# Optimization experiments

Measured on AMD Instinct MI355X. Metric: run time of the kernel, lower is better.

Reference implementation:

```python
import jax, jax.numpy as jnp
import numpy as np

L = 16       # flow_layers
B = 131072   # batch
D = 256      # z_dim
EPS = 1e-7


def setup_inputs() -> dict:
    key = jax.random.key(0)
    ks = jax.random.split(key, 7)
    z = jax.random.normal(ks[0], (B, D), dtype=jnp.float32)
    # match torch init ranges
    planar_w = jax.random.uniform(ks[1], (L, D), jnp.float32, -0.01, 0.01)
    planar_b = jax.random.uniform(ks[2], (L,), jnp.float32, -0.01, 0.01)
    planar_s = jax.random.uniform(ks[3], (L, D), jnp.float32, -0.01, 0.01)
    radial_z0 = jax.random.uniform(ks[4], (L, D), jnp.float32, -0.01, 0.01)
    radial_a = jax.random.uniform(ks[5], (L,), jnp.float32, 0.01, 1.0)
    radial_b = jax.random.uniform(ks[6], (L,), jnp.float32, -0.01, 0.01)
    return dict(z=z, planar_w=planar_w, planar_b=planar_b, planar_s=planar_s,
                radial_z0=radial_z0, radial_a=radial_a, radial_b=radial_b)


def reference(z, planar_w, planar_b, planar_s, radial_z0, radial_a, radial_b):
    # Faithful translation of AlternatingFlow._run_flow with train=True.
    # The torch .item() parameter corrections become predicated jnp.where updates.
    loss = jnp.zeros((z.shape[0],), dtype=z.dtype)
    for i in range(L):
        if i % 2 == 0:  # planar flow step
            w = planar_w[i]          # [D]
            b = planar_b[i]          # scalar
            s = planar_s[i]          # [D]
            margin = jnp.dot(s, w)   # scalar  (mm(scale, weight.T))
            comp = -1.0 + jnp.log1p(jnp.exp(margin)) - margin
            s = jnp.where(margin < -1.0, s + comp * w / jnp.linalg.norm(w), s)
            act = jnp.tanh(z @ w + b)                 # [B]
            z = z + s[None, :] * act[:, None]          # [B, D]
            psi_dot_s = (1.0 - act * act) * jnp.dot(w, s)  # psi @ s.T, [B]
            det = 1.0 + psi_dot_s
            loss = loss + jnp.log(jnp.abs(det) + EPS)
        else:  # radial flow step
            z0 = radial_z0[i]        # [D]
            a = radial_a[i]          # scalar
            beta = radial_b[i]       # scalar
            beta = jnp.where(beta < -a, -a + jnp.log1p(jnp.exp(beta)), beta)
            radius = z - z0[None, :]                   # [B, D]
            r = jnp.linalg.norm(radius, axis=1)        # [B], per-row norm
            h = 1.0 / (a + r)                          # [B]
            z = z + beta * h[:, None] * radius
            # NOTE: torch uses radius.norm(2) with no dim here -> scalar full-tensor norm
            R = jnp.linalg.norm(radius)                # scalar (faithful to original)
            diagonal = (1.0 + beta * h) ** (D - 1)
            det = diagonal * (1.0 + beta * h - beta * (h * h) * R)
            loss = loss + jnp.log(jnp.abs(det) + EPS)
    return z, jnp.mean(loss)
```

## Files before the change

kernel.cpp:

```cpp
#include <hip/hip_runtime.h>
#include <hip/hip_fp16.h>
#include <math.h>

#define B_ROWS 131072
#define DDIM 256
#define EPSF 1e-7f
#define NB1 4096
#define NWAVES (NB1 * 8)
#define NB3 512

#define PBW_OFF  0
#define RV_OFF   1179648
#define PL_OFF   1179712
#define PBRL_OFF 1179776
#define HW_OFF   1183872

__device__ __forceinline__ float uni(float x) {
    return __int_as_float(__builtin_amdgcn_readfirstlane(__float_as_int(x)));
}

#define DPP_ADD(v, ctrl)                                                        \
    (v) += __int_as_float(__builtin_amdgcn_update_dpp(                          \
               0, __float_as_int(v), (ctrl), 0xF, 0xF, true))

#define REDUCE16(v)                                                             \
    do {                                                                        \
        DPP_ADD(v, 0xB1);                             \
        DPP_ADD(v, 0x4E);                             \
        DPP_ADD(v, 0x124);                            \
        DPP_ADD(v, 0x128);                            \
    } while (0)

__global__ __launch_bounds__(512, 6) void k_main(
    const float* __restrict__ z_in, float* __restrict__ z_out,
    const float* __restrict__ pw, const float* __restrict__ pb,
    const float* __restrict__ ps, const float* __restrict__ rz0,
    const float* __restrict__ ra, const float* __restrict__ rb,
    __half* __restrict__ h_ws, float* __restrict__ pbw)
{
    __shared__ float swp[8 * DDIM];
    __shared__ float ssp[8 * DDIM];
    __shared__ float sz0[8 * DDIM];
    __shared__ float sscal[32];

    const int wave = threadIdx.x >> 6;
    const int lane = threadIdx.x & 63;

    {
        const int p = wave;
        const int ip = 2 * p, ir = 2 * p + 1;
        float4 wv  = ((const float4*)(pw  + ip * DDIM))[lane];
        float4 sv  = ((const float4*)(ps  + ip * DDIM))[lane];
        float4 z0v = ((const float4*)(rz0 + ir * DDIM))[lane];
        float m  = wv.x * sv.x + wv.y * sv.y + wv.z * sv.z + wv.w * sv.w;
        float n2 = wv.x * wv.x + wv.y * wv.y + wv.z * wv.z + wv.w * wv.w;
#pragma unroll
        for (int o = 1; o < 64; o <<= 1) {
            m  += __shfl_xor(m,  o, 64);
            n2 += __shfl_xor(n2, o, 64);
        }
        if (m < -1.0f) {
            float comp = -1.0f + log1pf(expf(m)) - m;
            float f = comp / sqrtf(n2);
            sv.x += f * wv.x; sv.y += f * wv.y; sv.z += f * wv.z; sv.w += f * wv.w;
        }
        float wd = wv.x * sv.x + wv.y * sv.y + wv.z * sv.z + wv.w * sv.w;
#pragma unroll
        for (int o = 1; o < 64; o <<= 1) wd += __shfl_xor(wd, o, 64);
        const int nd = ((lane & 3) << 6) | ((lane >> 2) << 2);
        *((float4*)(swp + p * DDIM + nd)) = wv;
        *((float4*)(ssp + p * DDIM + nd)) = sv;
        *((float4*)(sz0 + p * DDIM + nd)) = z0v;
        if (lane == 0) {
            sscal[p]      = pb[ip];
            sscal[8 + p]  = wd;
            float a = ra[ir], bt = rb[ir];
            if (bt < -a) bt = -a + log1pf(expf(bt));
            sscal[16 + p] = a;
            sscal[24 + p] = bt;
        }
    }
    __syncthreads();

    float pbv[8], wds[8], av[8], bv[8];
#pragma unroll
    for (int p = 0; p < 8; ++p) {
        pbv[p] = uni(sscal[p]);
        wds[p] = uni(sscal[8 + p]);
        av[p]  = uni(sscal[16 + p]);
        bv[p]  = uni(sscal[24 + p]);
    }

    const int g = lane >> 4;
    const int j = lane & 15;
    const int row = blockIdx.x * 32 + wave * 4 + g;

    float4 zv[4];
    {
        const float4* zp = (const float4*)(z_in + (size_t)row * DDIM + j * 16);
#pragma unroll
        for (int k = 0; k < 4; ++k) zv[k] = zp[k];
    }

    float r2s[8];
    float pls = 0.0f;
    unsigned hw32[4];

#pragma unroll
    for (int i = 0; i < 16; ++i) {
        if ((i & 1) == 0) {
            const int p = i >> 1;
            const float4* wb = ((const float4*)swp) + p * 64 + j;
            float t = 0.0f;
#pragma unroll
            for (int k = 0; k < 4; ++k) {
                float4 wv = wb[k * 16];
                t += zv[k].x * wv.x + zv[k].y * wv.y + zv[k].z * wv.z + zv[k].w * wv.w;
            }
            REDUCE16(t);
            float x = t + pbv[p];
            float e = __expf(2.0f * x);
            float act = 1.0f - 2.0f / (e + 1.0f);
            const float4* sb = ((const float4*)ssp) + p * 64 + j;
#pragma unroll
            for (int k = 0; k < 4; ++k) {
                float4 sv = sb[k * 16];
                zv[k].x += sv.x * act; zv[k].y += sv.y * act;
                zv[k].z += sv.z * act; zv[k].w += sv.w * act;
            }
            float det = 1.0f + (1.0f - act * act) * wds[p];
            pls += __logf(fabsf(det) + EPSF);
        } else {
            const int r = i >> 1;
            const float4* zb = ((const float4*)sz0) + r * 64 + j;
            float4 rd[4];
            float t = 0.0f;
#pragma unroll
            for (int k = 0; k < 4; ++k) {
                float4 zz = zb[k * 16];
                rd[k].x = zv[k].x - zz.x; rd[k].y = zv[k].y - zz.y;
                rd[k].z = zv[k].z - zz.z; rd[k].w = zv[k].w - zz.w;
                t += rd[k].x * rd[k].x + rd[k].y * rd[k].y
                   + rd[k].z * rd[k].z + rd[k].w * rd[k].w;
            }
            REDUCE16(t);
            float rr = sqrtf(t);
            float h = 1.0f / (av[r] + rr);
            float bh = bv[r] * h;
#pragma unroll
            for (int k = 0; k < 4; ++k) {
                zv[k].x += bh * rd[k].x; zv[k].y += bh * rd[k].y;
                zv[k].z += bh * rd[k].z; zv[k].w += bh * rd[k].w;
            }
            r2s[r] = t;
            unsigned hu = (unsigned)__half_as_ushort(__float2half(h));
            if ((r & 1) == 0) hw32[r >> 1] = hu;
            else              hw32[r >> 1] |= hu << 16;
        }
    }

    {
        float4* op = (float4*)(z_out + (size_t)row * DDIM + j * 16);
#pragma unroll
        for (int k = 0; k < 4; ++k) op[k] = zv[k];
        if (j == 0)
            ((uint4*)h_ws)[row] = make_uint4(hw32[0], hw32[1], hw32[2], hw32[3]);
    }

    const int waveId = blockIdx.x * 8 + wave;
#pragma unroll
    for (int q = 0; q < 9; ++q) {
        float v = (q < 8) ? r2s[q] : pls;
        if (j != 0) v = 0.0f;
        v += __shfl_xor(v, 16, 64);
        v += __shfl_xor(v, 32, 64);
        if (lane == 0) pbw[waveId * 9 + q] = v;
    }
}

__global__ __launch_bounds__(1024) void k_stats(
    const float* __restrict__ pbw, double* __restrict__ Rv, double* __restrict__ PL)
{
    __shared__ double sd[1024];
    const int q = blockIdx.x;
    const int t = threadIdx.x;
    double v = 0.0;
    for (int i = t; i < NWAVES; i += 1024) v += (double)pbw[i * 9 + q];
    sd[t] = v;
    __syncthreads();
#pragma unroll
    for (int off = 512; off > 0; off >>= 1) {
        if (t < off) sd[t] += sd[t + off];
        __syncthreads();
    }
    if (t == 0) {
        if (q < 8) Rv[q] = sqrt(sd[0]);
        else       PL[0] = sd[0];
    }
}

__global__ __launch_bounds__(256) void k_rloss(
    const __half* __restrict__ h_ws, const float* __restrict__ ra,
    const float* __restrict__ rb, const double* __restrict__ Rv,
    double* __restrict__ pb_rl)
{
    __shared__ double sd[256];
    __shared__ float sbeta[8], sR[8];
    if (threadIdx.x < 8) {
        int r = threadIdx.x;
        float a = ra[2 * r + 1], bt = rb[2 * r + 1];
        if (bt < -a) bt = -a + log1pf(expf(bt));
        sbeta[r] = bt;
        sR[r] = (float)Rv[r];
    }
    __syncthreads();
    const int row = blockIdx.x * 256 + threadIdx.x;
    uint4 hp = ((const uint4*)h_ws)[row];
    unsigned hw[4] = {hp.x, hp.y, hp.z, hp.w};
    double ls = 0.0;
#pragma unroll
    for (int r = 0; r < 8; ++r) {
        unsigned hu = (hw[r >> 1] >> ((r & 1) * 16)) & 0xFFFFu;
        float h = __half2float(__ushort_as_half((unsigned short)hu));
        float beta = sbeta[r];
        float bh = beta * h;
        float t1 = 1.0f + bh;
        float diag = exp2f(255.0f * __log2f(t1));
        float det = diag * (t1 - beta * h * h * sR[r]);
        ls += (double)__logf(fabsf(det) + EPSF);
    }
    sd[threadIdx.x] = ls;
    __syncthreads();
#pragma unroll
    for (int off = 128; off > 0; off >>= 1) {
        if (threadIdx.x < off) sd[threadIdx.x] += sd[threadIdx.x + off];
        __syncthreads();
    }
    if (threadIdx.x == 0) pb_rl[blockIdx.x] = sd[0];
}

__global__ __launch_bounds__(256) void k_final(
    const double* __restrict__ pb_rl, const double* __restrict__ PL,
    float* __restrict__ out_loss)
{
    __shared__ double sd[256];
    int t = threadIdx.x;
    double v = 0.0;
    for (int jj = t; jj < NB3; jj += 256) v += pb_rl[jj];
    sd[t] = v;
    __syncthreads();
#pragma unroll
    for (int off = 128; off > 0; off >>= 1) {
        if (t < off) sd[t] += sd[t + off];
        __syncthreads();
    }
    if (t == 0) out_loss[0] = (float)((sd[0] + PL[0]) / (double)B_ROWS);
}

extern "C" void kernel_launch(void* const* d_in, const int* in_sizes, int n_in,
                              void* d_out, int out_size, void* d_ws, size_t ws_size,
                              hipStream_t stream) {
    const float* z   = (const float*)d_in[0];
    const float* pw  = (const float*)d_in[1];
    const float* pb  = (const float*)d_in[2];
    const float* ps  = (const float*)d_in[3];
    const float* rz0 = (const float*)d_in[4];
    const float* ra  = (const float*)d_in[5];
    const float* rb  = (const float*)d_in[6];
    float* out = (float*)d_out;

    char* ws = (char*)d_ws;
    float*  pbw   = (float*)(ws + PBW_OFF);
    double* Rv    = (double*)(ws + RV_OFF);
    double* PL    = (double*)(ws + PL_OFF);
    double* pb_rl = (double*)(ws + PBRL_OFF);
    __half* h_ws  = (__half*)(ws + HW_OFF);

    k_main<<<NB1, 512, 0, stream>>>(z, out, pw, pb, ps, rz0, ra, rb, h_ws, pbw);
    k_stats<<<9, 1024, 0, stream>>>(pbw, Rv, PL);
    k_rloss<<<NB3, 256, 0, stream>>>(h_ws, ra, rb, Rv, pb_rl);
    k_final<<<1, 256, 0, stream>>>(pb_rl, PL, out + (size_t)B_ROWS * DDIM);
}
```

Measured before the change: 98.32 us.

## Process two row tiles per block and use fast rcp/sqrt intrinsics

Halves the grid so each block handles 64 rows in two sequential tiles. This amortizes the per-block parameter setup (loading flow weights into shared memory, the margin corrections, the scalar broadcasts) over twice the rows, and halves the partial-sum buffer that the stats kernel reduces. It also swaps the exact division and sqrt for the hardware rcp/sqrt/rsq intrinsics and splits the dot products into four independent partial sums for more ILP. The cost is fewer blocks available to hide memory latency, plus slightly lower numerical precision.

```diff
diff --git a/kernel.cpp b/kernel.cpp
--- a/kernel.cpp
+++ b/kernel.cpp
@@ -5,15 +5,15 @@
 #define B_ROWS 131072
 #define DDIM 256
 #define EPSF 1e-7f
-#define NB1 4096
+#define NB1 2048
 #define NWAVES (NB1 * 8)
 #define NB3 512
 
 #define PBW_OFF  0
-#define RV_OFF   1179648
-#define PL_OFF   1179712
-#define PBRL_OFF 1179776
-#define HW_OFF   1183872
+#define RV_OFF   589824
+#define PL_OFF   589888
+#define PBRL_OFF 589952
+#define HW_OFF   594048
 
 __device__ __forceinline__ float uni(float x) {
     return __int_as_float(__builtin_amdgcn_readfirstlane(__float_as_int(x)));
@@ -30,6 +30,90 @@
         DPP_ADD(v, 0x124);                            \
         DPP_ADD(v, 0x128);                            \
     } while (0)
+
+#define TILE_BODY(ROWBASE)                                                      \
+    {                                                                           \
+        const int row = (ROWBASE) + wave * 4 + g;                               \
+        float4 zv[4];                                                           \
+        {                                                                       \
+            const float4* zp = (const float4*)(z_in + (size_t)row * DDIM + j * 16); \
+            _Pragma("unroll")                                                   \
+            for (int k = 0; k < 4; ++k) zv[k] = zp[k];                          \
+        }                                                                       \
+        float pls = 0.0f;                                                       \
+        unsigned hw32[4];                                                       \
+        _Pragma("unroll")                                                       \
+        for (int i = 0; i < 16; ++i) {                                          \
+            if ((i & 1) == 0) {                                     \
+                const int p = i >> 1;                                           \
+                const float4* wb = ((const float4*)swp) + p * 64 + j;           \
+                float t0, t1, t2, t3;                                           \
+                {                                                               \
+                    float4 w0 = wb[0], w1 = wb[16], w2 = wb[32], w3 = wb[48];   \
+                    t0 = zv[0].x * w0.x + zv[0].y * w0.y + zv[0].z * w0.z + zv[0].w * w0.w; \
+                    t1 = zv[1].x * w1.x + zv[1].y * w1.y + zv[1].z * w1.z + zv[1].w * w1.w; \
+                    t2 = zv[2].x * w2.x + zv[2].y * w2.y + zv[2].z * w2.z + zv[2].w * w2.w; \
+                    t3 = zv[3].x * w3.x + zv[3].y * w3.y + zv[3].z * w3.z + zv[3].w * w3.w; \
+                }                                                               \
+                float t = (t0 + t1) + (t2 + t3);                                \
+                REDUCE16(t);                                                    \
+                float x = t + pbv[p];                                           \
+                float e = __expf(2.0f * x);                                     \
+                float act = 1.0f - 2.0f * __builtin_amdgcn_rcpf(e + 1.0f);      \
+                const float4* sb = ((const float4*)ssp) + p * 64 + j;           \
+                _Pragma("unroll")                                               \
+                for (int k = 0; k < 4; ++k) {                                   \
+                    float4 sv = sb[k * 16];                                     \
+                    zv[k].x += sv.x * act; zv[k].y += sv.y * act;               \
+                    zv[k].z += sv.z * act; zv[k].w += sv.w * act;               \
+                }                                                               \
+                float det = 1.0f + (1.0f - act * act) * wds[p];                 \
+                pls += __logf(fabsf(det) + EPSF);                               \
+            } else {                                                \
+                const int r = i >> 1;                                           \
+                const float4* zb = ((const float4*)sz0) + r * 64 + j;           \
+                float4 rd[4];                                                   \
+                float t0, t1, t2, t3;                                           \
+                {                                                               \
+                    float4 z0 = zb[0], z1 = zb[16], z2 = zb[32], z3 = zb[48];   \
+                    rd[0].x = zv[0].x - z0.x; rd[0].y = zv[0].y - z0.y;         \
+                    rd[0].z = zv[0].z - z0.z; rd[0].w = zv[0].w - z0.w;         \
+                    rd[1].x = zv[1].x - z1.x; rd[1].y = zv[1].y - z1.y;         \
+                    rd[1].z = zv[1].z - z1.z; rd[1].w = zv[1].w - z1.w;         \
+                    rd[2].x = zv[2].x - z2.x; rd[2].y = zv[2].y - z2.y;         \
+                    rd[2].z = zv[2].z - z2.z; rd[2].w = zv[2].w - z2.w;         \
+                    rd[3].x = zv[3].x - z3.x; rd[3].y = zv[3].y - z3.y;         \
+                    rd[3].z = zv[3].z - z3.z; rd[3].w = zv[3].w - z3.w;         \
+                    t0 = rd[0].x * rd[0].x + rd[0].y * rd[0].y + rd[0].z * rd[0].z + rd[0].w * rd[0].w; \
+                    t1 = rd[1].x * rd[1].x + rd[1].y * rd[1].y + rd[1].z * rd[1].z + rd[1].w * rd[1].w; \
+                    t2 = rd[2].x * rd[2].x + rd[2].y * rd[2].y + rd[2].z * rd[2].z + rd[2].w * rd[2].w; \
+                    t3 = rd[3].x * rd[3].x + rd[3].y * rd[3].y + rd[3].z * rd[3].z + rd[3].w * rd[3].w; \
+                }                                                               \
+                float t = (t0 + t1) + (t2 + t3);                                \
+                REDUCE16(t);                                                    \
+                float rr = __builtin_amdgcn_sqrtf(t);                           \
+                float h = __builtin_amdgcn_rcpf(av[r] + rr);                    \
+                float bh = bv[r] * h;                                           \
+                _Pragma("unroll")                                               \
+                for (int k = 0; k < 4; ++k) {                                   \
+                    zv[k].x += bh * rd[k].x; zv[k].y += bh * rd[k].y;           \
+                    zv[k].z += bh * rd[k].z; zv[k].w += bh * rd[k].w;           \
+                }                                                               \
+                acc_ss[r] += (j == 0) ? t : 0.0f;                               \
+                unsigned hu = (unsigned)__half_as_ushort(__float2half(h));      \
+                if ((r & 1) == 0) hw32[r >> 1] = hu;                            \
+                else              hw32[r >> 1] |= hu << 16;                     \
+            }                                                                   \
+        }                                                                       \
+        acc_pl += (j == 0) ? pls : 0.0f;                                        \
+        {                                                                       \
+            float4* op = (float4*)(z_out + (size_t)row * DDIM + j * 16);        \
+            _Pragma("unroll")                                                   \
+            for (int k = 0; k < 4; ++k) op[k] = zv[k];                          \
+            if (j == 0)                                                         \
+                ((uint4*)h_ws)[row] = make_uint4(hw32[0], hw32[1], hw32[2], hw32[3]); \
+        }                                                                       \
+    }
 
 __global__ __launch_bounds__(512, 6) void k_main(
     const float* __restrict__ z_in, float* __restrict__ z_out,
@@ -61,7 +145,7 @@
         }
         if (m < -1.0f) {
             float comp = -1.0f + log1pf(expf(m)) - m;
-            float f = comp / sqrtf(n2);
+            float f = comp * __builtin_amdgcn_rsqf(n2);
             sv.x += f * wv.x; sv.y += f * wv.y; sv.z += f * wv.z; sv.w += f * wv.w;
         }
         float wd = wv.x * sv.x + wv.y * sv.y + wv.z * sv.z + wv.w * sv.w;
@@ -93,85 +177,20 @@
 
     const int g = lane >> 4;
     const int j = lane & 15;
-    const int row = blockIdx.x * 32 + wave * 4 + g;
-
-    float4 zv[4];
-    {
-        const float4* zp = (const float4*)(z_in + (size_t)row * DDIM + j * 16);
-#pragma unroll
-        for (int k = 0; k < 4; ++k) zv[k] = zp[k];
-    }
-
-    float r2s[8];
-    float pls = 0.0f;
-    unsigned hw32[4];
-
-#pragma unroll
-    for (int i = 0; i < 16; ++i) {
-        if ((i & 1) == 0) {
-            const int p = i >> 1;
-            const float4* wb = ((const float4*)swp) + p * 64 + j;
-            float t = 0.0f;
-#pragma unroll
-            for (int k = 0; k < 4; ++k) {
-                float4 wv = wb[k * 16];
-                t += zv[k].x * wv.x + zv[k].y * wv.y + zv[k].z * wv.z + zv[k].w * wv.w;
-            }
-            REDUCE16(t);
-            float x = t + pbv[p];
-            float e = __expf(2.0f * x);
-            float act = 1.0f - 2.0f / (e + 1.0f);
-            const float4* sb = ((const float4*)ssp) + p * 64 + j;
-#pragma unroll
-            for (int k = 0; k < 4; ++k) {
-                float4 sv = sb[k * 16];
-                zv[k].x += sv.x * act; zv[k].y += sv.y * act;
-                zv[k].z += sv.z * act; zv[k].w += sv.w * act;
-            }
-            float det = 1.0f + (1.0f - act * act) * wds[p];
-            pls += __logf(fabsf(det) + EPSF);
-        } else {
-            const int r = i >> 1;
-            const float4* zb = ((const float4*)sz0) + r * 64 + j;
-            float4 rd[4];
-            float t = 0.0f;
-#pragma unroll
-            for (int k = 0; k < 4; ++k) {
-                float4 zz = zb[k * 16];
-                rd[k].x = zv[k].x - zz.x; rd[k].y = zv[k].y - zz.y;
-                rd[k].z = zv[k].z - zz.z; rd[k].w = zv[k].w - zz.w;
-                t += rd[k].x * rd[k].x + rd[k].y * rd[k].y
-                   + rd[k].z * rd[k].z + rd[k].w * rd[k].w;
-            }
-            REDUCE16(t);
-            float rr = sqrtf(t);
-            float h = 1.0f / (av[r] + rr);
-            float bh = bv[r] * h;
-#pragma unroll
-            for (int k = 0; k < 4; ++k) {
-                zv[k].x += bh * rd[k].x; zv[k].y += bh * rd[k].y;
-                zv[k].z += bh * rd[k].z; zv[k].w += bh * rd[k].w;
-            }
-            r2s[r] = t;
-            unsigned hu = (unsigned)__half_as_ushort(__float2half(h));
-            if ((r & 1) == 0) hw32[r >> 1] = hu;
-            else              hw32[r >> 1] |= hu << 16;
-        }
-    }
-
-    {
-        float4* op = (float4*)(z_out + (size_t)row * DDIM + j * 16);
-#pragma unroll
-        for (int k = 0; k < 4; ++k) op[k] = zv[k];
-        if (j == 0)
-            ((uint4*)h_ws)[row] = make_uint4(hw32[0], hw32[1], hw32[2], hw32[3]);
-    }
+
+    float acc_ss[8];
+#pragma unroll
+    for (int q = 0; q < 8; ++q) acc_ss[q] = 0.0f;
+    float acc_pl = 0.0f;
+
+    const int rowbase = blockIdx.x * 64;
+    TILE_BODY(rowbase)
+    TILE_BODY(rowbase + 32)
 
     const int waveId = blockIdx.x * 8 + wave;
 #pragma unroll
     for (int q = 0; q < 9; ++q) {
-        float v = (q < 8) ? r2s[q] : pls;
-        if (j != 0) v = 0.0f;
+        float v = (q < 8) ? acc_ss[q] : acc_pl;
         v += __shfl_xor(v, 16, 64);
         v += __shfl_xor(v, 32, 64);
         if (lane == 0) pbw[waveId * 9 + q] = v;
```

Measured after the change: 111.7 us. 1.14x slower.

## Process two rows per lane group to reuse LDS parameter loads

Applied to the files above, without the earlier changes.

Each 16-lane group now carries two rows (A and B) through all 16 flow steps. This halves the number of blocks and the LDS reads of w, s and z0 per row, and gives two independent reduction chains for more instruction-level parallelism. It also switches to hardware rcp/rsq/sqrt intrinsics and lowers the occupancy hint to 4 blocks per CU to make room for the doubled register state. Workspace offsets are shrunk to match the halved wave count. Lower occupancy may hide memory latency less well, and the approximate intrinsics slightly change numerics.

```diff
diff --git a/kernel.cpp b/kernel.cpp
--- a/kernel.cpp
+++ b/kernel.cpp
@@ -5,15 +5,15 @@
 #define B_ROWS 131072
 #define DDIM 256
 #define EPSF 1e-7f
-#define NB1 4096
+#define NB1 2048
 #define NWAVES (NB1 * 8)
 #define NB3 512
 
 #define PBW_OFF  0
-#define RV_OFF   1179648
-#define PL_OFF   1179712
-#define PBRL_OFF 1179776
-#define HW_OFF   1183872
+#define RV_OFF   589824
+#define PL_OFF   589888
+#define PBRL_OFF 589952
+#define HW_OFF   594048
 
 __device__ __forceinline__ float uni(float x) {
     return __int_as_float(__builtin_amdgcn_readfirstlane(__float_as_int(x)));
@@ -31,7 +31,7 @@
         DPP_ADD(v, 0x128);                            \
     } while (0)
 
-__global__ __launch_bounds__(512, 6) void k_main(
+__global__ __launch_bounds__(512, 4) void k_main(
     const float* __restrict__ z_in, float* __restrict__ z_out,
     const float* __restrict__ pw, const float* __restrict__ pb,
     const float* __restrict__ ps, const float* __restrict__ rz0,
@@ -61,7 +61,7 @@
         }
         if (m < -1.0f) {
             float comp = -1.0f + log1pf(expf(m)) - m;
-            float f = comp / sqrtf(n2);
+            float f = comp * __builtin_amdgcn_rsqf(n2);
             sv.x += f * wv.x; sv.y += f * wv.y; sv.z += f * wv.z; sv.w += f * wv.w;
         }
         float wd = wv.x * sv.x + wv.y * sv.y + wv.z * sv.z + wv.w * sv.w;
@@ -93,85 +93,115 @@
 
     const int g = lane >> 4;
     const int j = lane & 15;
-    const int row = blockIdx.x * 32 + wave * 4 + g;
-
-    float4 zv[4];
+    const int rowA = blockIdx.x * 64 + wave * 8 + g;
+    const int rowB = rowA + 4;
+
+    float4 zvA[4], zvB[4];
     {
-        const float4* zp = (const float4*)(z_in + (size_t)row * DDIM + j * 16);
-#pragma unroll
-        for (int k = 0; k < 4; ++k) zv[k] = zp[k];
-    }
-
-    float r2s[8];
-    float pls = 0.0f;
-    unsigned hw32[4];
+        const float4* zpA = (const float4*)(z_in + (size_t)rowA * DDIM + j * 16);
+        const float4* zpB = (const float4*)(z_in + (size_t)rowB * DDIM + j * 16);
+#pragma unroll
+        for (int k = 0; k < 4; ++k) { zvA[k] = zpA[k]; zvB[k] = zpB[k]; }
+    }
+
+    float acc_ss[8];
+    float acc_pl = 0.0f;
+    unsigned hwA[4], hwB[4];
 
 #pragma unroll
     for (int i = 0; i < 16; ++i) {
         if ((i & 1) == 0) {
             const int p = i >> 1;
             const float4* wb = ((const float4*)swp) + p * 64 + j;
-            float t = 0.0f;
-#pragma unroll
-            for (int k = 0; k < 4; ++k) {
-                float4 wv = wb[k * 16];
-                t += zv[k].x * wv.x + zv[k].y * wv.y + zv[k].z * wv.z + zv[k].w * wv.w;
-            }
-            REDUCE16(t);
-            float x = t + pbv[p];
-            float e = __expf(2.0f * x);
-            float act = 1.0f - 2.0f / (e + 1.0f);
+            float4 w0 = wb[0], w1 = wb[16], w2 = wb[32], w3 = wb[48];
+            float tA0 = zvA[0].x * w0.x + zvA[0].y * w0.y + zvA[0].z * w0.z + zvA[0].w * w0.w;
+            float tB0 = zvB[0].x * w0.x + zvB[0].y * w0.y + zvB[0].z * w0.z + zvB[0].w * w0.w;
+            float tA1 = zvA[1].x * w1.x + zvA[1].y * w1.y + zvA[1].z * w1.z + zvA[1].w * w1.w;
+            float tB1 = zvB[1].x * w1.x + zvB[1].y * w1.y + zvB[1].z * w1.z + zvB[1].w * w1.w;
+            float tA2 = zvA[2].x * w2.x + zvA[2].y * w2.y + zvA[2].z * w2.z + zvA[2].w * w2.w;
+            float tB2 = zvB[2].x * w2.x + zvB[2].y * w2.y + zvB[2].z * w2.z + zvB[2].w * w2.w;
+            float tA3 = zvA[3].x * w3.x + zvA[3].y * w3.y + zvA[3].z * w3.z + zvA[3].w * w3.w;
+            float tB3 = zvB[3].x * w3.x + zvB[3].y * w3.y + zvB[3].z * w3.z + zvB[3].w * w3.w;
+            float tA = (tA0 + tA1) + (tA2 + tA3);
+            float tB = (tB0 + tB1) + (tB2 + tB3);
+            REDUCE16(tA);
+            REDUCE16(tB);
+            float xA = tA + pbv[p], xB = tB + pbv[p];
+            float eA = __expf(2.0f * xA), eB = __expf(2.0f * xB);
+            float actA = 1.0f - 2.0f * __builtin_amdgcn_rcpf(eA + 1.0f);
+            float actB = 1.0f - 2.0f * __builtin_amdgcn_rcpf(eB + 1.0f);
             const float4* sb = ((const float4*)ssp) + p * 64 + j;
-#pragma unroll
-            for (int k = 0; k < 4; ++k) {
-                float4 sv = sb[k * 16];
-                zv[k].x += sv.x * act; zv[k].y += sv.y * act;
-                zv[k].z += sv.z * act; zv[k].w += sv.w * act;
-            }
-            float det = 1.0f + (1.0f - act * act) * wds[p];
-            pls += __logf(fabsf(det) + EPSF);
+            float4 s0 = sb[0], s1 = sb[16], s2 = sb[32], s3 = sb[48];
+            zvA[0].x += s0.x * actA; zvA[0].y += s0.y * actA; zvA[0].z += s0.z * actA; zvA[0].w += s0.w * actA;
+            zvB[0].x += s0.x * actB; zvB[0].y += s0.y * actB; zvB[0].z += s0.z * actB; zvB[0].w += s0.w * actB;
+            zvA[1].x += s1.x * actA; zvA[1].y += s1.y * actA; zvA[1].z += s1.z * actA; zvA[1].w += s1.w * actA;
+            zvB[1].x += s1.x * actB; zvB[1].y += s1.y * actB; zvB[1].z += s1.z * actB; zvB[1].w += s1.w * actB;
+            zvA[2].x += s2.x * actA; zvA[2].y += s2.y * actA; zvA[2].z += s2.z * actA; zvA[2].w += s2.w * actA;
+            zvB[2].x += s2.x * actB; zvB[2].y += s2.y * actB; zvB[2].z += s2.z * actB; zvB[2].w += s2.w * actB;
+            zvA[3].x += s3.x * actA; zvA[3].y += s3.y * actA; zvA[3].z += s3.z * actA; zvA[3].w += s3.w * actA;
+            zvB[3].x += s3.x * actB; zvB[3].y += s3.y * actB; zvB[3].z += s3.z * actB; zvB[3].w += s3.w * actB;
+            float detA = 1.0f + (1.0f - actA * actA) * wds[p];
+            float detB = 1.0f + (1.0f - actB * actB) * wds[p];
+            acc_pl += (j == 0) ? (__logf(fabsf(detA) + EPSF) + __logf(fabsf(detB) + EPSF)) : 0.0f;
         } else {
             const int r = i >> 1;
             const float4* zb = ((const float4*)sz0) + r * 64 + j;
-            float4 rd[4];
-            float t = 0.0f;
+            float4 z0 = zb[0], z1 = zb[16], z2 = zb[32], z3 = zb[48];
+            float4 rdA[4], rdB[4];
+            rdA[0].x = zvA[0].x - z0.x; rdA[0].y = zvA[0].y - z0.y; rdA[0].z = zvA[0].z - z0.z; rdA[0].w = zvA[0].w - z0.w;
+            rdB[0].x = zvB[0].x - z0.x; rdB[0].y = zvB[0].y - z0.y; rdB[0].z = zvB[0].z - z0.z; rdB[0].w = zvB[0].w - z0.w;
+            rdA[1].x = zvA[1].x - z1.x; rdA[1].y = zvA[1].y - z1.y; rdA[1].z = zvA[1].z - z1.z; rdA[1].w = zvA[1].w - z1.w;
+            rdB[1].x = zvB[1].x - z1.x; rdB[1].y = zvB[1].y - z1.y; rdB[1].z = zvB[1].z - z1.z; rdB[1].w = zvB[1].w - z1.w;
+            rdA[2].x = zvA[2].x - z2.x; rdA[2].y = zvA[2].y - z2.y; rdA[2].z = zvA[2].z - z2.z; rdA[2].w = zvA[2].w - z2.w;
+            rdB[2].x = zvB[2].x - z2.x; rdB[2].y = zvB[2].y - z2.y; rdB[2].z = zvB[2].z - z2.z; rdB[2].w = zvB[2].w - z2.w;
+            rdA[3].x = zvA[3].x - z3.x; rdA[3].y = zvA[3].y - z3.y; rdA[3].z = zvA[3].z - z3.z; rdA[3].w = zvA[3].w - z3.w;
+            rdB[3].x = zvB[3].x - z3.x; rdB[3].y = zvB[3].y - z3.y; rdB[3].z = zvB[3].z - z3.z; rdB[3].w = zvB[3].w - z3.w;
+            float tA0 = rdA[0].x * rdA[0].x + rdA[0].y * rdA[0].y + rdA[0].z * rdA[0].z + rdA[0].w * rdA[0].w;
+            float tB0 = rdB[0].x * rdB[0].x + rdB[0].y * rdB[0].y + rdB[0].z * rdB[0].z + rdB[0].w * rdB[0].w;
+            float tA1 = rdA[1].x * rdA[1].x + rdA[1].y * rdA[1].y + rdA[1].z * rdA[1].z + rdA[1].w * rdA[1].w;
+            float tB1 = rdB[1].x * rdB[1].x + rdB[1].y * rdB[1].y + rdB[1].z * rdB[1].z + rdB[1].w * rdB[1].w;
+            float tA2 = rdA[2].x * rdA[2].x + rdA[2].y * rdA[2].y + rdA[2].z * rdA[2].z + rdA[2].w * rdA[2].w;
+            float tB2 = rdB[2].x * rdB[2].x + rdB[2].y * rdB[2].y + rdB[2].z * rdB[2].z + rdB[2].w * rdB[2].w;
+            float tA3 = rdA[3].x * rdA[3].x + rdA[3].y * rdA[3].y + rdA[3].z * rdA[3].z + rdA[3].w * rdA[3].w;
+            float tB3 = rdB[3].x * rdB[3].x + rdB[3].y * rdB[3].y + rdB[3].z * rdB[3].z + rdB[3].w * rdB[3].w;
+            float tA = (tA0 + tA1) + (tA2 + tA3);
+            float tB = (tB0 + tB1) + (tB2 + tB3);
+            REDUCE16(tA);
+            REDUCE16(tB);
+            float rrA = __builtin_amdgcn_sqrtf(tA), rrB = __builtin_amdgcn_sqrtf(tB);
+            float hA = __builtin_amdgcn_rcpf(av[r] + rrA);
+            float hB = __builtin_amdgcn_rcpf(av[r] + rrB);
+            float bhA = bv[r] * hA, bhB = bv[r] * hB;
 #pragma unroll
             for (int k = 0; k < 4; ++k) {
-                float4 zz = zb[k * 16];
-                rd[k].x = zv[k].x - zz.x; rd[k].y = zv[k].y - zz.y;
-                rd[k].z = zv[k].z - zz.z; rd[k].w = zv[k].w - zz.w;
-                t += rd[k].x * rd[k].x + rd[k].y * rd[k].y
-                   + rd[k].z * rd[k].z + rd[k].w * rd[k].w;
+                zvA[k].x += bhA * rdA[k].x; zvA[k].y += bhA * rdA[k].y;
+                zvA[k].z += bhA * rdA[k].z; zvA[k].w += bhA * rdA[k].w;
+                zvB[k].x += bhB * rdB[k].x; zvB[k].y += bhB * rdB[k].y;
+                zvB[k].z += bhB * rdB[k].z; zvB[k].w += bhB * rdB[k].w;
             }
-            REDUCE16(t);
-            float rr = sqrtf(t);
-            float h = 1.0f / (av[r] + rr);
-            float bh = bv[r] * h;
-#pragma unroll
-            for (int k = 0; k < 4; ++k) {
-                zv[k].x += bh * rd[k].x; zv[k].y += bh * rd[k].y;
-                zv[k].z += bh * rd[k].z; zv[k].w += bh * rd[k].w;
-            }
-            r2s[r] = t;
-            unsigned hu = (unsigned)__half_as_ushort(__float2half(h));
-            if ((r & 1) == 0) hw32[r >> 1] = hu;
-            else              hw32[r >> 1] |= hu << 16;
+            acc_ss[r] = (j == 0) ? (tA + tB) : 0.0f;
+            unsigned huA = (unsigned)__half_as_ushort(__float2half(hA));
+            unsigned huB = (unsigned)__half_as_ushort(__float2half(hB));
+            if ((r & 1) == 0) { hwA[r >> 1] = huA;        hwB[r >> 1] = huB; }
+            else              { hwA[r >> 1] |= huA << 16; hwB[r >> 1] |= huB << 16; }
         }
     }
 
     {
-        float4* op = (float4*)(z_out + (size_t)row * DDIM + j * 16);
-#pragma unroll
-        for (int k = 0; k < 4; ++k) op[k] = zv[k];
-        if (j == 0)
-            ((uint4*)h_ws)[row] = make_uint4(hw32[0], hw32[1], hw32[2], hw32[3]);
+        float4* opA = (float4*)(z_out + (size_t)rowA * DDIM + j * 16);
+        float4* opB = (float4*)(z_out + (size_t)rowB * DDIM + j * 16);
+#pragma unroll
+        for (int k = 0; k < 4; ++k) { opA[k] = zvA[k]; opB[k] = zvB[k]; }
+        if (j == 0) {
+            ((uint4*)h_ws)[rowA] = make_uint4(hwA[0], hwA[1], hwA[2], hwA[3]);
+            ((uint4*)h_ws)[rowB] = make_uint4(hwB[0], hwB[1], hwB[2], hwB[3]);
+        }
     }
 
     const int waveId = blockIdx.x * 8 + wave;
 #pragma unroll
     for (int q = 0; q < 9; ++q) {
-        float v = (q < 8) ? r2s[q] : pls;
-        if (j != 0) v = 0.0f;
+        float v = (q < 8) ? acc_ss[q] : acc_pl;
         v += __shfl_xor(v, 16, 64);
         v += __shfl_xor(v, 32, 64);
         if (lane == 0) pbw[waveId * 9 + q] = v;
```

New measurement: 98.04 us. Within noise of the previous version (-0.3%).
